# Kernel optimization log

Measured on AMD Instinct MI355X. Metric: run time of the kernel, lower is better.

The kernel has to match this reference:

```python
import jax, jax.numpy as jnp
import numpy as np

B, C_IN, N, F_OUT = 16, 128, 2048, 64
NEG_SLOPE = 0.33
MASK_VAL = -9e15


def setup_inputs() -> dict:
    key = jax.random.key(0)
    k1, k2, k3, k4 = jax.random.split(key, 4)
    h = jax.random.normal(k1, (B, C_IN, N, 1), dtype=jnp.float32)
    g = jax.random.normal(k2, (B, 1, N, N), dtype=jnp.float32)
    # xavier_uniform with gain=1.414
    gain = 1.414
    lim_W = gain * np.sqrt(6.0 / (C_IN + F_OUT))
    W = jax.random.uniform(k3, (C_IN, F_OUT), minval=-lim_W, maxval=lim_W, dtype=jnp.float32)
    lim_a = gain * np.sqrt(6.0 / (2 * F_OUT + 1))
    a = jax.random.uniform(k4, (2 * F_OUT, 1), minval=-lim_a, maxval=lim_a, dtype=jnp.float32)
    return {"h": h, "g": g, "W": W, "a": a}


def reference(h, g, W, a):
    # h: [B, C, N, 1] -> node features [B, N, C]
    hn = jnp.transpose(h[..., 0], (0, 2, 1))
    Wh = jnp.einsum('bnc,cf->bnf', hn, W)  # [B, N, F]
    F = W.shape[1]
    a1, a2 = a[:F, 0], a[F:, 0]
    # additive attention: e[i,j] = leakyrelu(Wh[i]@a1 + Wh[j]@a2)
    e = jax.nn.leaky_relu((Wh @ a1)[:, :, None] + (Wh @ a2)[:, None, :], NEG_SLOPE)  # [B,N,N]
    mask = g[:, 0] > 0  # [B, N, N]
    attn = jax.nn.softmax(jnp.where(mask, e, MASK_VAL), axis=-1)
    h_prime = jnp.einsum('bij,bjf->bif', attn, Wh)  # [B, N, F]
    return jnp.transpose(h_prime, (0, 2, 1))[..., None]  # [B, F, N, 1]
```

## Files before the change

kernel.cpp:

```cpp
#include <hip/hip_runtime.h>
#include <hip/hip_bf16.h>

#define NB 16
#define NC 128
#define NN 2048
#define NF 64
#define NEG_SLOPE 0.33f
#define EXP_K 1.4426950408889634f

typedef float    f32x2 __attribute__((ext_vector_type(2)));
typedef float    f32x4 __attribute__((ext_vector_type(4)));
typedef _Float16 f16x2 __attribute__((ext_vector_type(2)));
typedef _Float16 f16x4 __attribute__((ext_vector_type(4)));
typedef _Float16 f16x8 __attribute__((ext_vector_type(8)));

__device__ __forceinline__ float lrelu(float x) {
    return fmaxf(x, x * NEG_SLOPE);
}

__global__ __launch_bounds__(256) void k_precompute(
    const float* __restrict__ h, const float* __restrict__ W,
    const float* __restrict__ a, _Float16* __restrict__ wht,
    float* __restrict__ s1g, float* __restrict__ s2g)
{
    __shared__ float Wl[64 * 64];
    __shared__ float ht[64 * 129];

    const int t = threadIdx.x;
    const int b = blockIdx.x >> 5;
    const int n0 = (blockIdx.x & 31) << 6;
    const int lane = t & 63, cg = t >> 6;

    #pragma unroll 8
    for (int k = 0; k < 32; ++k) {
        const int c = cg * 32 + k;
        ht[lane * 129 + c] = h[(size_t)(b * NC + c) * NN + n0 + lane];
    }

    const int fg = t & 15, ns = t >> 4;
    f32x4 acc[4] = {};
    for (int half = 0; half < 2; ++half) {
        if (half) __syncthreads();
        #pragma unroll
        for (int k = 0; k < 4; ++k) {
            const int idx = k * 1024 + t * 4;
            *(f32x4*)&Wl[idx] = *(const f32x4*)&W[half * 4096 + idx];
        }
        __syncthreads();
        #pragma unroll 4
        for (int c2 = 0; c2 < 64; ++c2) {
            const f32x4 wv = *(const f32x4*)&Wl[c2 * 64 + fg * 4];
            #pragma unroll
            for (int m = 0; m < 4; ++m) {
                const float hv = ht[(ns * 4 + m) * 129 + half * 64 + c2];
                acc[m] += wv * hv;
            }
        }
    }

    const f32x4 a1v = *(const f32x4*)&a[fg * 4];
    const f32x4 a2v = *(const f32x4*)&a[NF + fg * 4];
    #pragma unroll
    for (int m = 0; m < 4; ++m) {
        float p1 = acc[m].x * a1v.x + acc[m].y * a1v.y + acc[m].z * a1v.z + acc[m].w * a1v.w;
        float p2 = acc[m].x * a2v.x + acc[m].y * a2v.y + acc[m].z * a2v.z + acc[m].w * a2v.w;
        #pragma unroll
        for (int d = 1; d < 16; d <<= 1) {
            p1 += __shfl_xor(p1, d, 64);
            p2 += __shfl_xor(p2, d, 64);
        }
        if (fg == 0) {
            const int n = n0 + ns * 4 + m;
            s1g[(size_t)b * NN + n] = p1;
            s2g[(size_t)b * NN + n] = p2;
        }
    }
    #pragma unroll
    for (int q = 0; q < 4; ++q) {
        f16x4 v;
        v[0] = (_Float16)acc[0][q]; v[1] = (_Float16)acc[1][q];
        v[2] = (_Float16)acc[2][q]; v[3] = (_Float16)acc[3][q];
        const int f = fg * 4 + q;
        *(f16x4*)&wht[((size_t)b * NF + f) * NN + n0 + ns * 4] = v;
    }
}

#define K2_N_HI    2
#define K2_N_STRIP 64
#define K2_N_XCD   8
__global__ __launch_bounds__(256, 2) void k_attn(
    const float* __restrict__ g, const _Float16* __restrict__ wht,
    const float* __restrict__ s1g, const float* __restrict__ s2g,
    float* __restrict__ out)
{
    __shared__ float s2b[NN];
    __shared__ float s1b[32];
    __shared__ float wred[4];
    __shared__ __align__(16) _Float16 Pc[4][1024];
    __shared__ f32x4 accS[2][5][64];

    const int t = threadIdx.x;
    const int lane = t & 63;
    const int w = t >> 6;
    const int rg = w & 1, jq = w >> 1;

    const int p = blockIdx.x;
    const int b = (p & 7) + ((p >> 9) << 3);
    const int strip = (p >> 3) & 63;
    const int i0 = strip * 32 + rg * 16;

    f32x4 sA = *(const f32x4*)&s2g[(size_t)b * NN + t * 8];
    f32x4 sB = *(const f32x4*)&s2g[(size_t)b * NN + t * 8 + 4];
    sA *= EXP_K; sB *= EXP_K;
    *(f32x4*)&s2b[t * 8] = sA;
    *(f32x4*)&s2b[t * 8 + 4] = sB;
    if (t < 32) s1b[t] = s1g[(size_t)b * NN + strip * 32 + t] * EXP_K;
    float lm = fmaxf(fmaxf(fmaxf(sA.x, sA.y), fmaxf(sA.z, sA.w)),
                     fmaxf(fmaxf(sB.x, sB.y), fmaxf(sB.z, sB.w)));
    #pragma unroll
    for (int d = 1; d < 64; d <<= 1) lm = fmaxf(lm, __shfl_xor(lm, d, 64));
    if (lane == 0) wred[w] = lm;
    __syncthreads();
    const float S2MAX = fmaxf(fmaxf(wred[0], wred[1]), fmaxf(wred[2], wred[3]));

    const int rh = lane >> 5;
    const int cp = lane & 31;
    float s1u[8], Mu[8];
    #pragma unroll
    for (int u = 0; u < 8; ++u) {
        const float v = s1b[rg * 16 + u * 2 + rh];
        s1u[u] = v;
        Mu[u]  = lrelu(v + S2MAX);
    }

    const float* gp = g + (size_t)b * NN * NN + (size_t)i0 * NN + jq * 1024 + cp * 2;
    const int fc = lane & 15, kg = lane >> 4;
    const _Float16* wb = wht + ((size_t)b * NF + fc) * NN + jq * 1024 + kg * 8;
    char* pcb = (char*)&Pc[w][0];

    f32x4 acc0 = {0,0,0,0}, acc1 = {0,0,0,0}, acc2 = {0,0,0,0}, acc3 = {0,0,0,0};
    f32x4 acc_s = {0,0,0,0};
    f16x8 ones;
    #pragma unroll
    for (int u = 0; u < 8; ++u) ones[u] = (_Float16)1.0f;

    f32x2 gA[8], gB[8], gC[8];
    #pragma unroll
    for (int u = 0; u < 8; ++u) gA[u] = *(const f32x2*)(gp + (size_t)(u * 2 + rh) * NN);
    #pragma unroll
    for (int u = 0; u < 8; ++u) gB[u] = *(const f32x2*)(gp + (size_t)(u * 2 + rh) * NN + 64);

#define CHUNK_BODY(CH, CUR, PF)                                                \
    {                                                                          \
        const int ch_ = (CH);                                                  \
         \
        f16x8 bfv[2][4];                                                       \
        _Pragma("unroll")                                                      \
        for (int ks = 0; ks < 2; ++ks) {                                       \
            _Pragma("unroll")                                                  \
            for (int ft = 0; ft < 4; ++ft)                                     \
                bfv[ks][ft] = *(const f16x8*)(wb + (size_t)ft * 16 * NN        \
                                              + ch_ * 64 + ks * 32);           \
        }                                                                      \
        __builtin_amdgcn_sched_barrier(0);                                     \
         \
        if (ch_ < 14) {                                                        \
            _Pragma("unroll")                                                  \
            for (int u = 0; u < 8; ++u)                                        \
                PF[u] = *(const f32x2*)(gp + (size_t)(u * 2 + rh) * NN         \
                                        + (ch_ + 2) * 64);                     \
        }                                                                      \
                   \
        const f32x2 sv = *(const f32x2*)&s2b[jq * 1024 + ch_ * 64 + cp * 2];   \
        _Pragma("unroll")                                                      \
        for (int u = 0; u < 8; ++u) {                                          \
            const int row = u * 2 + rh;                                        \
            const float p0 = (CUR[u].x > 0.0f)                                 \
                ? __builtin_amdgcn_exp2f(lrelu(s1u[u] + sv.x) - Mu[u]) : 0.0f; \
            const float p1 = (CUR[u].y > 0.0f)                                 \
                ? __builtin_amdgcn_exp2f(lrelu(s1u[u] + sv.y) - Mu[u]) : 0.0f; \
            f16x2 pv; pv[0] = (_Float16)p0; pv[1] = (_Float16)p1;              \
            *(f16x2*)(pcb + ((row * 128 + cp * 4) ^ ((row & 7) << 4))) = pv;   \
        }                                                                      \
                      \
        _Pragma("unroll")                                                      \
        for (int ks = 0; ks < 2; ++ks) {                                       \
            const f16x8 af = *(const f16x8*)(pcb +                             \
                ((fc * 128 + ks * 64 + kg * 16) ^ ((fc & 7) << 4)));           \
            acc0  = __builtin_amdgcn_mfma_f32_16x16x32_f16(af, bfv[ks][0], acc0, 0, 0, 0); \
            acc1  = __builtin_amdgcn_mfma_f32_16x16x32_f16(af, bfv[ks][1], acc1, 0, 0, 0); \
            acc2  = __builtin_amdgcn_mfma_f32_16x16x32_f16(af, bfv[ks][2], acc2, 0, 0, 0); \
            acc3  = __builtin_amdgcn_mfma_f32_16x16x32_f16(af, bfv[ks][3], acc3, 0, 0, 0); \
            acc_s = __builtin_amdgcn_mfma_f32_16x16x32_f16(af, ones,       acc_s, 0, 0, 0); \
        }                                                                      \
    }

    #pragma unroll 1
    for (int c = 0; c < 15; c += 3) {
        CHUNK_BODY(c,     gA, gC);
        CHUNK_BODY(c + 1, gB, gA);
        CHUNK_BODY(c + 2, gC, gB);
    }
    CHUNK_BODY(15, gA, gC);
#undef CHUNK_BODY

    if (jq == 1) {
        accS[rg][0][lane] = acc0;
        accS[rg][1][lane] = acc1;
        accS[rg][2][lane] = acc2;
        accS[rg][3][lane] = acc3;
        accS[rg][4][lane] = acc_s;
    }
    __syncthreads();
    if (jq == 0) {
        acc0  += accS[rg][0][lane];
        acc1  += accS[rg][1][lane];
        acc2  += accS[rg][2][lane];
        acc3  += accS[rg][3][lane];
        acc_s += accS[rg][4][lane];
        f32x4 rinv;
        #pragma unroll
        for (int q = 0; q < 4; ++q) rinv[q] = 1.0f / acc_s[q];

        const size_t ob = ((size_t)b * NF + fc) * NN + (size_t)i0 + kg * 4;
        f32x4 o0, o1, o2, o3;
        #pragma unroll
        for (int q = 0; q < 4; ++q) {
            o0[q] = acc0[q] * rinv[q];
            o1[q] = acc1[q] * rinv[q];
            o2[q] = acc2[q] * rinv[q];
            o3[q] = acc3[q] * rinv[q];
        }
        *(f32x4*)&out[ob]                   = o0;
        *(f32x4*)&out[ob + (size_t)16 * NN] = o1;
        *(f32x4*)&out[ob + (size_t)32 * NN] = o2;
        *(f32x4*)&out[ob + (size_t)48 * NN] = o3;
    }
}

extern "C" void kernel_launch(void* const* d_in, const int* in_sizes, int n_in,
                              void* d_out, int out_size, void* d_ws, size_t ws_size,
                              hipStream_t stream)
{
    (void)in_sizes; (void)n_in; (void)out_size; (void)ws_size;
    const float* h = (const float*)d_in[0];
    const float* g = (const float*)d_in[1];
    const float* W = (const float*)d_in[2];
    const float* a = (const float*)d_in[3];
    float* out = (float*)d_out;

    char* ws = (char*)d_ws;
    _Float16* wht = (_Float16*)ws;
    float* s1 = (float*)(ws + (size_t)NB * NF * NN * sizeof(_Float16));
    float* s2 = s1 + (size_t)NB * NN;

    k_precompute<<<NB * (NN / 64), 256, 0, stream>>>(h, W, a, wht, s1, s2);
    k_attn<<<K2_N_HI * K2_N_STRIP * K2_N_XCD, 256, 0, stream>>>(g, wht, s1, s2, out);
}
```

Measured before the change: 98.25 us.

## Precompute adjacency mask as bitmask in separate kernel, drop g prefetch pipeline

Adds a k_mask kernel that reads the full fp32 adjacency g once and packs the g>0 test into 32-bit words per lane. The attention kernel then loads 8 mask words up front and tests bits, instead of streaming and triple-buffering fp32 g values through registers. This cuts register pressure and removes the manual prefetch pipeline from k_attn. The cost is an extra kernel launch and the same full read of g (256MB) in k_mask, plus a small mask write and read back, with no overlap against the attention compute.

```diff
diff --git a/kernel.cpp b/kernel.cpp
--- a/kernel.cpp
+++ b/kernel.cpp
@@ -85,11 +85,39 @@
     }
 }
 
+__global__ __launch_bounds__(256) void k_mask(
+    const float* __restrict__ g, unsigned* __restrict__ maskW)
+{
+    const int lane = threadIdx.x & 63;
+    const int rh = lane >> 5;
+    const int cp = lane & 31;
+    const int wid = (blockIdx.x * blockDim.x + threadIdx.x) >> 6;
+    const int totw = (gridDim.x * blockDim.x) >> 6;
+    const int NPAIR = NB * NN / 2;
+
+    for (int rp = wid; rp < NPAIR; rp += totw) {
+        const int grow = rp * 2 + rh;
+        const float* gr = g + (size_t)grow * NN + cp * 2;
+        unsigned w0 = 0, w1 = 0;
+        #pragma unroll
+        for (int ch = 0; ch < 16; ++ch) {
+            const f32x2 a  = *(const f32x2*)(gr + ch * 64);
+            const f32x2 b2 = *(const f32x2*)(gr + 1024 + ch * 64);
+            w0 |= (a.x  > 0.0f ? 1u : 0u) << (2 * ch);
+            w0 |= (a.y  > 0.0f ? 1u : 0u) << (2 * ch + 1);
+            w1 |= (b2.x > 0.0f ? 1u : 0u) << (2 * ch);
+            w1 |= (b2.y > 0.0f ? 1u : 0u) << (2 * ch + 1);
+        }
+        maskW[((size_t)grow * 2 + 0) * 32 + cp] = w0;
+        maskW[((size_t)grow * 2 + 1) * 32 + cp] = w1;
+    }
+}
+
 #define K2_N_HI    2
 #define K2_N_STRIP 64
 #define K2_N_XCD   8
 __global__ __launch_bounds__(256, 2) void k_attn(
-    const float* __restrict__ g, const _Float16* __restrict__ wht,
+    const unsigned* __restrict__ maskW, const _Float16* __restrict__ wht,
     const float* __restrict__ s1g, const float* __restrict__ s2g,
     float* __restrict__ out)
 {
@@ -120,11 +148,17 @@
     #pragma unroll
     for (int d = 1; d < 64; d <<= 1) lm = fmaxf(lm, __shfl_xor(lm, d, 64));
     if (lane == 0) wred[w] = lm;
+
+    const int rh = lane >> 5;
+    const int cp = lane & 31;
+    unsigned mw[8];
+    #pragma unroll
+    for (int u = 0; u < 8; ++u)
+        mw[u] = maskW[((size_t)(b * NN + i0 + u * 2 + rh) * 2 + jq) * 32 + cp];
+
     __syncthreads();
     const float S2MAX = fmaxf(fmaxf(wred[0], wred[1]), fmaxf(wred[2], wred[3]));
 
-    const int rh = lane >> 5;
-    const int cp = lane & 31;
     float s1u[8], Mu[8];
     #pragma unroll
     for (int u = 0; u < 8; ++u) {
@@ -133,7 +167,6 @@
         Mu[u]  = lrelu(v + S2MAX);
     }
 
-    const float* gp = g + (size_t)b * NN * NN + (size_t)i0 * NN + jq * 1024 + cp * 2;
     const int fc = lane & 15, kg = lane >> 4;
     const _Float16* wb = wht + ((size_t)b * NF + fc) * NN + jq * 1024 + kg * 8;
     char* pcb = (char*)&Pc[w][0];
@@ -144,65 +177,37 @@
     #pragma unroll
     for (int u = 0; u < 8; ++u) ones[u] = (_Float16)1.0f;
 
-    f32x2 gA[8], gB[8], gC[8];
-    #pragma unroll
-    for (int u = 0; u < 8; ++u) gA[u] = *(const f32x2*)(gp + (size_t)(u * 2 + rh) * NN);
-    #pragma unroll
-    for (int u = 0; u < 8; ++u) gB[u] = *(const f32x2*)(gp + (size_t)(u * 2 + rh) * NN + 64);
-
-#define CHUNK_BODY(CH, CUR, PF)                                                \
-    {                                                                          \
-        const int ch_ = (CH);                                                  \
-         \
-        f16x8 bfv[2][4];                                                       \
-        _Pragma("unroll")                                                      \
-        for (int ks = 0; ks < 2; ++ks) {                                       \
-            _Pragma("unroll")                                                  \
-            for (int ft = 0; ft < 4; ++ft)                                     \
-                bfv[ks][ft] = *(const f16x8*)(wb + (size_t)ft * 16 * NN        \
-                                              + ch_ * 64 + ks * 32);           \
-        }                                                                      \
-        __builtin_amdgcn_sched_barrier(0);                                     \
-         \
-        if (ch_ < 14) {                                                        \
-            _Pragma("unroll")                                                  \
-            for (int u = 0; u < 8; ++u)                                        \
-                PF[u] = *(const f32x2*)(gp + (size_t)(u * 2 + rh) * NN         \
-                                        + (ch_ + 2) * 64);                     \
-        }                                                                      \
-                   \
-        const f32x2 sv = *(const f32x2*)&s2b[jq * 1024 + ch_ * 64 + cp * 2];   \
-        _Pragma("unroll")                                                      \
-        for (int u = 0; u < 8; ++u) {                                          \
-            const int row = u * 2 + rh;                                        \
-            const float p0 = (CUR[u].x > 0.0f)                                 \
-                ? __builtin_amdgcn_exp2f(lrelu(s1u[u] + sv.x) - Mu[u]) : 0.0f; \
-            const float p1 = (CUR[u].y > 0.0f)                                 \
-                ? __builtin_amdgcn_exp2f(lrelu(s1u[u] + sv.y) - Mu[u]) : 0.0f; \
-            f16x2 pv; pv[0] = (_Float16)p0; pv[1] = (_Float16)p1;              \
-            *(f16x2*)(pcb + ((row * 128 + cp * 4) ^ ((row & 7) << 4))) = pv;   \
-        }                                                                      \
-                      \
-        _Pragma("unroll")                                                      \
-        for (int ks = 0; ks < 2; ++ks) {                                       \
-            const f16x8 af = *(const f16x8*)(pcb +                             \
-                ((fc * 128 + ks * 64 + kg * 16) ^ ((fc & 7) << 4)));           \
-            acc0  = __builtin_amdgcn_mfma_f32_16x16x32_f16(af, bfv[ks][0], acc0, 0, 0, 0); \
-            acc1  = __builtin_amdgcn_mfma_f32_16x16x32_f16(af, bfv[ks][1], acc1, 0, 0, 0); \
-            acc2  = __builtin_amdgcn_mfma_f32_16x16x32_f16(af, bfv[ks][2], acc2, 0, 0, 0); \
-            acc3  = __builtin_amdgcn_mfma_f32_16x16x32_f16(af, bfv[ks][3], acc3, 0, 0, 0); \
-            acc_s = __builtin_amdgcn_mfma_f32_16x16x32_f16(af, ones,       acc_s, 0, 0, 0); \
-        }                                                                      \
-    }
-
-    #pragma unroll 1
-    for (int c = 0; c < 15; c += 3) {
-        CHUNK_BODY(c,     gA, gC);
-        CHUNK_BODY(c + 1, gB, gA);
-        CHUNK_BODY(c + 2, gC, gB);
-    }
-    CHUNK_BODY(15, gA, gC);
-#undef CHUNK_BODY
+    for (int ch = 0; ch < 16; ++ch) {
+        f16x8 bfv[2][4];
+        #pragma unroll
+        for (int ks = 0; ks < 2; ++ks) {
+            #pragma unroll
+            for (int ft = 0; ft < 4; ++ft)
+                bfv[ks][ft] = *(const f16x8*)(wb + (size_t)ft * 16 * NN + ch * 64 + ks * 32);
+        }
+        const f32x2 sv = *(const f32x2*)&s2b[jq * 1024 + ch * 64 + cp * 2];
+        #pragma unroll
+        for (int u = 0; u < 8; ++u) {
+            const int row = u * 2 + rh;
+            const unsigned bits = mw[u] >> (2 * ch);
+            const float p0 = (bits & 1u)
+                ? __builtin_amdgcn_exp2f(lrelu(s1u[u] + sv.x) - Mu[u]) : 0.0f;
+            const float p1 = (bits & 2u)
+                ? __builtin_amdgcn_exp2f(lrelu(s1u[u] + sv.y) - Mu[u]) : 0.0f;
+            f16x2 pv; pv[0] = (_Float16)p0; pv[1] = (_Float16)p1;
+            *(f16x2*)(pcb + ((row * 128 + cp * 4) ^ ((row & 7) << 4))) = pv;
+        }
+        #pragma unroll
+        for (int ks = 0; ks < 2; ++ks) {
+            const f16x8 af = *(const f16x8*)(pcb +
+                ((fc * 128 + ks * 64 + kg * 16) ^ ((fc & 7) << 4)));
+            acc0  = __builtin_amdgcn_mfma_f32_16x16x32_f16(af, bfv[ks][0], acc0, 0, 0, 0);
+            acc1  = __builtin_amdgcn_mfma_f32_16x16x32_f16(af, bfv[ks][1], acc1, 0, 0, 0);
+            acc2  = __builtin_amdgcn_mfma_f32_16x16x32_f16(af, bfv[ks][2], acc2, 0, 0, 0);
+            acc3  = __builtin_amdgcn_mfma_f32_16x16x32_f16(af, bfv[ks][3], acc3, 0, 0, 0);
+            acc_s = __builtin_amdgcn_mfma_f32_16x16x32_f16(af, ones,       acc_s, 0, 0, 0);
+        }
+    }
 
     if (jq == 1) {
         accS[rg][0][lane] = acc0;
@@ -253,7 +258,9 @@
     _Float16* wht = (_Float16*)ws;
     float* s1 = (float*)(ws + (size_t)NB * NF * NN * sizeof(_Float16));
     float* s2 = s1 + (size_t)NB * NN;
-
+    unsigned* maskW = (unsigned*)(s2 + (size_t)NB * NN);
+
+    k_mask<<<2048, 256, 0, stream>>>(g, maskW);
     k_precompute<<<NB * (NN / 64), 256, 0, stream>>>(h, W, a, wht, s1, s2);
-    k_attn<<<K2_N_HI * K2_N_STRIP * K2_N_XCD, 256, 0, stream>>>(g, wht, s1, s2, out);
-}
+    k_attn<<<K2_N_HI * K2_N_STRIP * K2_N_XCD, 256, 0, stream>>>(maskW, wht, s1, s2, out);
+}
```

Measured after the change: 122.0 us. +24.2%, slower.
